# Kernel optimization log

Measured on AMD Instinct MI355X. Metric: run time of the kernel, lower is better.

Reference implementation:

```python
import jax, jax.numpy as jnp
import numpy as np

N = 50000
E = 800000
B = 8  # number of graphs


def gcn_conv(x, src, dst, W, b, n_nodes):
    # PyG GCNConv: add self-loops, symmetric deg^{-1/2} normalization,
    # linear transform, scatter-add aggregation at dst, then bias.
    loops = jnp.arange(n_nodes, dtype=src.dtype)
    s = jnp.concatenate([src, loops])
    d = jnp.concatenate([dst, loops])
    deg = jax.ops.segment_sum(jnp.ones_like(d, dtype=x.dtype), d, num_segments=n_nodes)
    dinv = jnp.where(deg > 0, jax.lax.rsqrt(deg), 0.0)
    norm = dinv[s] * dinv[d]                      # [E+N]
    xw = x @ W                                    # [N, out]
    msg = xw[s] * norm[:, None]                   # gather + scale
    out = jax.ops.segment_sum(msg, d, num_segments=n_nodes)  # scatter-add
    return out + b


def global_attention(x, batch, gate_w, gate_b, n_graphs):
    gate = x @ gate_w + gate_b                    # [N, 1]
    gmax = jax.ops.segment_max(gate, batch, num_segments=n_graphs)
    gmax = jnp.where(jnp.isfinite(gmax), gmax, 0.0)
    e = jnp.exp(gate - gmax[batch])               # segment-stable softmax
    denom = jax.ops.segment_sum(e, batch, num_segments=n_graphs)
    alpha = e / denom[batch]                      # [N, 1]
    return jax.ops.segment_sum(alpha * x, batch, num_segments=n_graphs)  # [B, d]


def setup_inputs() -> dict:
    key = jax.random.key(0)
    ks = jax.random.split(key, 10)
    x = jax.random.normal(ks[0], (N, 512), dtype=jnp.float32)
    edge_index = jax.random.randint(ks[1], (2, E), 0, N, dtype=jnp.int32)
    batch = jnp.sort(jax.random.randint(ks[2], (N,), 0, B, dtype=jnp.int32))
    W1 = jax.random.normal(ks[3], (512, 256), dtype=jnp.float32) / np.sqrt(512)
    b1 = jnp.zeros((256,), dtype=jnp.float32)
    W2 = jax.random.normal(ks[4], (256, 256), dtype=jnp.float32) / np.sqrt(256)
    b2 = jnp.zeros((256,), dtype=jnp.float32)
    gate_w = jax.random.normal(ks[5], (256, 1), dtype=jnp.float32) / np.sqrt(256)
    gate_b = jnp.zeros((1,), dtype=jnp.float32)
    return {"x": x, "edge_index": edge_index, "batch": batch,
            "W1": W1, "b1": b1, "W2": W2, "b2": b2,
            "gate_w": gate_w, "gate_b": gate_b}


def reference(x, edge_index, batch, W1, b1, W2, b2, gate_w, gate_b):
    src, dst = edge_index[0], edge_index[1]
    h = jax.nn.relu(gcn_conv(x, src, dst, W1, b1, N))
    h = jax.nn.relu(gcn_conv(h, src, dst, W2, b2, N))
    return global_attention(h, batch, gate_w, gate_b, B)
```

## Files before the change

kernel.cpp:

```cpp
#include <hip/hip_runtime.h>
#include <hip/hip_bf16.h>
#include <math.h>

#define FDIM 256
#define CAP 64
#define NGRAPH 8
#define GMAX_BLOCKS 64
#define FINAL_BLOCKS 512

typedef __attribute__((ext_vector_type(8))) short bf16x8;
typedef __attribute__((ext_vector_type(4))) float f32x4;
typedef __attribute__((ext_vector_type(2))) float f32x2;

__device__ __forceinline__ unsigned enc_f(float x){
  unsigned u = __float_as_uint(x);
  return (u >> 31) ? ~u : (u | 0x80000000u);
}
__device__ __forceinline__ float dec_f(unsigned u){
  return (u >> 31) ? __uint_as_float(u & 0x7FFFFFFFu) : __uint_as_float(~u);
}

__device__ __forceinline__ unsigned short f2bf(float f){
  unsigned u = __float_as_uint(f);
  unsigned r = (u + 0x7FFFu + ((u >> 16) & 1u)) >> 16;
  return (unsigned short)r;
}
__device__ __forceinline__ float bf2f(unsigned short h){
  return __uint_as_float(((unsigned)h) << 16);
}
__device__ __forceinline__ unsigned pk2(float a, float b){
  return (unsigned)f2bf(a) | ((unsigned)f2bf(b) << 16);
}
__device__ __forceinline__ unsigned char f2fp8(float v){
  unsigned p = __builtin_amdgcn_cvt_pk_fp8_f32(v, v, 0u, false);
  return (unsigned char)(p & 0xFFu);
}

__global__ void init_k(int* cnt, float* denom, float* out, int N){
  int i = blockIdx.x * blockDim.x + threadIdx.x;
  if (i < N) cnt[i] = 0;
  if (i < NGRAPH) denom[i] = 0.f;
  if (i < NGRAPH * FDIM) out[i] = 0.f;
}

__global__ void csr_k(const int* __restrict__ src, const int* __restrict__ dst,
                      int* __restrict__ cnt, int* __restrict__ col, int E){
  int e = blockIdx.x * blockDim.x + threadIdx.x;
  if (e < E){
    int d = dst[e];
    int pos = atomicAdd(&cnt[d], 1);
    if (pos < CAP) col[(size_t)d * CAP + pos] = src[e];
  }
}

__global__ void dinv_k(const int* __restrict__ cnt, float* __restrict__ dinv, int N){
  int i = blockIdx.x * blockDim.x + threadIdx.x;
  if (i < N) dinv[i] = rsqrtf((float)(cnt[i] + 1));
}

__global__ void wconv_k(const float* __restrict__ W1, const float* __restrict__ W2,
                        unsigned short* __restrict__ Wt1, unsigned short* __restrict__ Wt2){
  int idx = blockIdx.x * 256 + threadIdx.x;
  if (idx < 512 * 256){
    int k = idx >> 8, n = idx & 255;
    Wt1[(size_t)n * 512 + k] = f2bf(W1[idx]);
  } else {
    int j = idx - 512 * 256;
    if (j < 256 * 256){
      int k = j >> 8, n = j & 255;
      Wt2[(size_t)n * 256 + k] = f2bf(W2[j]);
    }
  }
}

template<int K, bool A_FP32>
__global__ __launch_bounds__(512) void gemm_k(const void* __restrict__ Av,
                                              const unsigned short* __restrict__ Bt,
                                              unsigned char* __restrict__ C, int M){
  __shared__ unsigned short As[128 * 64];
  __shared__ unsigned short Bs[256 * 64];
  const int tid = threadIdx.x;
  const int lane = tid & 63, wid = tid >> 6;
  const int wr = wid >> 2, wc = wid & 3;
  const int m0 = blockIdx.x * 128;
  f32x4 acc[4][4] = {};

  float4 arf0, arf1, arf2, arf3;
  uint4  arb0, arb1;
  uint4  brg0, brg1, brg2, brg3;

  const int rA0 = tid >> 3,          kqA0 = tid & 7;
  const int rA1 = (512 + tid) >> 3,  kqA1 = tid & 7;

  auto issue = [&](int k0){
    if (A_FP32){
      const float* A = (const float*)Av;
      const float* p0 = A + (size_t)min(m0 + rA0, M - 1) * K + k0 + kqA0 * 8;
      const float* p1 = A + (size_t)min(m0 + rA1, M - 1) * K + k0 + kqA1 * 8;
      arf0 = *(const float4*)p0; arf1 = *(const float4*)(p0 + 4);
      arf2 = *(const float4*)p1; arf3 = *(const float4*)(p1 + 4);
    } else {
      const unsigned short* A = (const unsigned short*)Av;
      arb0 = *(const uint4*)(A + (size_t)min(m0 + rA0, M - 1) * K + k0 + kqA0 * 8);
      arb1 = *(const uint4*)(A + (size_t)min(m0 + rA1, M - 1) * K + k0 + kqA1 * 8);
    }
    {
      int n0 = tid >> 3, n1 = (512 + tid) >> 3, n2 = (1024 + tid) >> 3, n3 = (1536 + tid) >> 3;
      int kq = tid & 7;
      brg0 = *(const uint4*)(Bt + (size_t)n0 * K + k0 + kq * 8);
      brg1 = *(const uint4*)(Bt + (size_t)n1 * K + k0 + kq * 8);
      brg2 = *(const uint4*)(Bt + (size_t)n2 * K + k0 + kq * 8);
      brg3 = *(const uint4*)(Bt + (size_t)n3 * K + k0 + kq * 8);
    }
  };

  auto writeLDS = [&](){
    int kq = tid & 7;
    {
      uint4 u0, u1;
      if (A_FP32){
        u0.x = pk2(arf0.x, arf0.y); u0.y = pk2(arf0.z, arf0.w);
        u0.z = pk2(arf1.x, arf1.y); u0.w = pk2(arf1.z, arf1.w);
        u1.x = pk2(arf2.x, arf2.y); u1.y = pk2(arf2.z, arf2.w);
        u1.z = pk2(arf3.x, arf3.y); u1.w = pk2(arf3.z, arf3.w);
      } else { u0 = arb0; u1 = arb1; }
      *(uint4*)((char*)As + ((rA0 * 128 + kq * 16) ^ ((rA0 & 7) << 4))) = u0;
      *(uint4*)((char*)As + ((rA1 * 128 + kq * 16) ^ ((rA1 & 7) << 4))) = u1;
    }
    {
      int n0 = tid >> 3, n1 = (512 + tid) >> 3, n2 = (1024 + tid) >> 3, n3 = (1536 + tid) >> 3;
      *(uint4*)((char*)Bs + ((n0 * 128 + kq * 16) ^ ((n0 & 7) << 4))) = brg0;
      *(uint4*)((char*)Bs + ((n1 * 128 + kq * 16) ^ ((n1 & 7) << 4))) = brg1;
      *(uint4*)((char*)Bs + ((n2 * 128 + kq * 16) ^ ((n2 & 7) << 4))) = brg2;
      *(uint4*)((char*)Bs + ((n3 * 128 + kq * 16) ^ ((n3 & 7) << 4))) = brg3;
    }
  };

  issue(0);
  for (int k0 = 0; k0 < K; k0 += 64){
    writeLDS();
    __syncthreads();
    if (k0 + 64 < K) issue(k0 + 64);

    #pragma unroll
    for (int kk = 0; kk < 64; kk += 32){
      bf16x8 af[4], bfr[4];
      int kb = kk * 2 + ((lane >> 4) << 4);
      #pragma unroll
      for (int mi = 0; mi < 4; ++mi){
        int r = wr * 64 + mi * 16 + (lane & 15);
        af[mi] = *(bf16x8*)((char*)As + ((r * 128 + kb) ^ ((r & 7) << 4)));
      }
      #pragma unroll
      for (int ni = 0; ni < 4; ++ni){
        int n = wc * 64 + ni * 16 + (lane & 15);
        bfr[ni] = *(bf16x8*)((char*)Bs + ((n * 128 + kb) ^ ((n & 7) << 4)));
      }
      #pragma unroll
      for (int mi = 0; mi < 4; ++mi)
        #pragma unroll
        for (int ni = 0; ni < 4; ++ni)
          acc[mi][ni] = __builtin_amdgcn_mfma_f32_16x16x32_bf16(af[mi], bfr[ni], acc[mi][ni], 0, 0, 0);
    }
    __syncthreads();
  }

  #pragma unroll
  for (int mi = 0; mi < 4; ++mi){
    #pragma unroll
    for (int reg = 0; reg < 4; ++reg){
      int row = m0 + wr * 64 + mi * 16 + ((lane >> 4) << 2) + reg;
      if (row < M){
        #pragma unroll
        for (int ni = 0; ni < 4; ++ni){
          int colc = wc * 64 + ni * 16 + (lane & 15);
          C[(size_t)row * FDIM + colc] = f2fp8(acc[mi][ni][reg]);
        }
      }
    }
  }
}

template<bool GATE>
__global__ __launch_bounds__(256) void agg_k(const unsigned char* __restrict__ xw,
                                             const float* __restrict__ dinv,
                                             const int* __restrict__ col,
                                             const int* __restrict__ cnt,
                                             const float* __restrict__ bias,
                                             unsigned short* __restrict__ outb,
                                             const float* __restrict__ gw,
                                             const float* __restrict__ gb,
                                             float* __restrict__ gate, int N){
  int node = blockIdx.x * 4 + (threadIdx.x >> 6);
  if (node >= N) return;
  int lane = threadIdx.x & 63;
  float di = dinv[node];
  int n = min(cnt[node], CAP);
  int s = 0; float w = 0.f;
  if (lane < n){ s = col[(size_t)node * CAP + lane]; w = di * dinv[s]; }

  float a0, a1, a2, a3;
  {
    unsigned u = *(const unsigned*)(xw + (size_t)node * FDIM + lane * 4);
    f32x2 lo = __builtin_amdgcn_cvt_pk_f32_fp8(u, false);
    f32x2 hi = __builtin_amdgcn_cvt_pk_f32_fp8(u, true);
    float sw = di * di;
    a0 = sw * lo.x; a1 = sw * lo.y; a2 = sw * hi.x; a3 = sw * hi.y;
  }

  unsigned bufA[8], bufB[8];
  int nc = (n + 7) >> 3;

  auto loadChunk = [&](unsigned (&buf)[8], int c){
    #pragma unroll
    for (int j = 0; j < 8; ++j){
      int e = c * 8 + j;
      int se = __shfl(s, e);
      buf[j] = *(const unsigned*)(xw + (size_t)se * FDIM + lane * 4);
    }
  };
  auto consChunk = [&](unsigned (&buf)[8], int c){
    #pragma unroll
    for (int j = 0; j < 8; ++j){
      int e = c * 8 + j;
      float we = __shfl(w, e);
      f32x2 lo = __builtin_amdgcn_cvt_pk_f32_fp8(buf[j], false);
      f32x2 hi = __builtin_amdgcn_cvt_pk_f32_fp8(buf[j], true);
      a0 += we * lo.x; a1 += we * lo.y;
      a2 += we * hi.x; a3 += we * hi.y;
    }
  };

  if (nc > 0) loadChunk(bufA, 0);
  for (int c = 0; c < nc; ++c){
    if (c & 1){
      if (c + 1 < nc) loadChunk(bufA, c + 1);
      consChunk(bufB, c);
    } else {
      if (c + 1 < nc) loadChunk(bufB, c + 1);
      consChunk(bufA, c);
    }
  }

  float4 bv = *(const float4*)(bias + lane * 4);
  a0 = fmaxf(a0 + bv.x, 0.f); a1 = fmaxf(a1 + bv.y, 0.f);
  a2 = fmaxf(a2 + bv.z, 0.f); a3 = fmaxf(a3 + bv.w, 0.f);
  {
    ushort4 r = make_ushort4(f2bf(a0), f2bf(a1), f2bf(a2), f2bf(a3));
    *(ushort4*)(outb + (size_t)node * FDIM + lane * 4) = r;
  }
  if (GATE){
    float4 g = *(const float4*)(gw + lane * 4);
    float val = a0 * g.x + a1 * g.y + a2 * g.z + a3 * g.w;
    #pragma unroll
    for (int off = 32; off; off >>= 1) val += __shfl_down(val, off);
    if (lane == 0) gate[node] = val + gb[0];
  }
}

__global__ __launch_bounds__(256) void gmax_k(const float* __restrict__ gate,
                                              const int* __restrict__ batch,
                                              unsigned* __restrict__ pmax, int N){
  __shared__ unsigned smax[NGRAPH];
  int tid = threadIdx.x;
  if (tid < NGRAPH) smax[tid] = 0u;
  __syncthreads();
  int chunk = (N + gridDim.x - 1) / gridDim.x;
  int begin = blockIdx.x * chunk;
  int end = min(begin + chunk, N);
  int curg = -1; unsigned curm = 0u;
  for (int i = begin + tid; i < end; i += 256){
    int g = batch[i];
    unsigned v = enc_f(gate[i]);
    if (g != curg){
      if (curg >= 0) atomicMax(&smax[curg], curm);
      curg = g; curm = v;
    } else if (v > curm) curm = v;
  }
  if (curg >= 0) atomicMax(&smax[curg], curm);
  __syncthreads();
  if (tid < NGRAPH) pmax[blockIdx.x * NGRAPH + tid] = smax[tid];
}

__global__ __launch_bounds__(256) void denom_k(float* __restrict__ gate,
                                               const int* __restrict__ batch,
                                               const unsigned* __restrict__ pmax,
                                               float* __restrict__ denom, int N){
  __shared__ unsigned sge[NGRAPH];
  __shared__ float gm[NGRAPH];
  __shared__ float dsum[NGRAPH];
  int tid = threadIdx.x;
  if (tid < NGRAPH){ sge[tid] = 0u; dsum[tid] = 0.f; }
  __syncthreads();
  for (int j = tid; j < GMAX_BLOCKS * NGRAPH; j += 256)
    atomicMax(&sge[j & (NGRAPH - 1)], pmax[j]);
  __syncthreads();
  if (tid < NGRAPH){
    unsigned u = sge[tid];
    gm[tid] = (u == 0u) ? 0.f : dec_f(u);
  }
  __syncthreads();
  int chunk = (N + gridDim.x - 1) / gridDim.x;
  int begin = blockIdx.x * chunk;
  int end = min(begin + chunk, N);
  int curg = -1; float cursum = 0.f;
  for (int i = begin + tid; i < end; i += 256){
    int g = batch[i];
    float e = expf(gate[i] - gm[g]);
    gate[i] = e;
    if (g != curg){
      if (curg >= 0) atomicAdd(&dsum[curg], cursum);
      curg = g; cursum = e;
    } else cursum += e;
  }
  if (curg >= 0) atomicAdd(&dsum[curg], cursum);
  __syncthreads();
  if (tid < NGRAPH && dsum[tid] != 0.f) atomicAdd(&denom[tid], dsum[tid]);
}

__global__ __launch_bounds__(256) void final_k(const unsigned short* __restrict__ h,
                                               const float* __restrict__ e,
                                               const int* __restrict__ batch,
                                               const float* __restrict__ denom,
                                               float* __restrict__ out, int N){
  __shared__ float sacc[NGRAPH * FDIM];
  int tid = threadIdx.x;
  #pragma unroll
  for (int j = tid; j < NGRAPH * FDIM; j += 256) sacc[j] = 0.f;
  __syncthreads();
  int lane = tid & 63, w = tid >> 6;
  int chunk = (N + gridDim.x - 1) / gridDim.x;
  int begin = blockIdx.x * chunk;
  int end = min(begin + chunk, N);
  float4 acc = make_float4(0.f, 0.f, 0.f, 0.f);
  int curg = -1;
  for (int i = begin + w; i < end; i += 4){
    int g = batch[i];
    if (g != curg){
      if (curg >= 0){
        atomicAdd(&sacc[curg * FDIM + lane * 4 + 0], acc.x);
        atomicAdd(&sacc[curg * FDIM + lane * 4 + 1], acc.y);
        atomicAdd(&sacc[curg * FDIM + lane * 4 + 2], acc.z);
        atomicAdd(&sacc[curg * FDIM + lane * 4 + 3], acc.w);
        acc = make_float4(0.f, 0.f, 0.f, 0.f);
      }
      curg = g;
    }
    float alpha = e[i] / denom[g];
    ushort4 v = *(const ushort4*)(h + (size_t)i * FDIM + lane * 4);
    acc.x += alpha * bf2f(v.x); acc.y += alpha * bf2f(v.y);
    acc.z += alpha * bf2f(v.z); acc.w += alpha * bf2f(v.w);
  }
  if (curg >= 0){
    atomicAdd(&sacc[curg * FDIM + lane * 4 + 0], acc.x);
    atomicAdd(&sacc[curg * FDIM + lane * 4 + 1], acc.y);
    atomicAdd(&sacc[curg * FDIM + lane * 4 + 2], acc.z);
    atomicAdd(&sacc[curg * FDIM + lane * 4 + 3], acc.w);
  }
  __syncthreads();
  if (begin < end){
    int g0 = batch[begin], g1 = batch[end - 1];
    for (int g = g0; g <= g1; ++g){
      float v = sacc[g * FDIM + tid];
      if (v != 0.f) atomicAdd(&out[g * FDIM + tid], v);
    }
  }
}

extern "C" void kernel_launch(void* const* d_in, const int* in_sizes, int n_in,
                              void* d_out, int out_size, void* d_ws, size_t ws_size,
                              hipStream_t stream){
  const float* x     = (const float*)d_in[0];
  const int*   ei    = (const int*)  d_in[1];
  const int*   batch = (const int*)  d_in[2];
  const float* W1    = (const float*)d_in[3];
  const float* b1    = (const float*)d_in[4];
  const float* W2    = (const float*)d_in[5];
  const float* b2    = (const float*)d_in[6];
  const float* gw    = (const float*)d_in[7];
  const float* gb    = (const float*)d_in[8];
  float* out = (float*)d_out;

  const int N = in_sizes[2];
  const int E = in_sizes[1] / 2;
  const int* src = ei;
  const int* dst = ei + E;

  size_t off = 0;
  auto carve = [&](size_t bytes) -> void* {
    void* p = (char*)d_ws + off;
    off += (bytes + 255) / 256 * 256;
    return p;
  };
  unsigned short* h     = (unsigned short*)carve((size_t)N * FDIM * 2);
  unsigned short* h1b   = (unsigned short*)carve((size_t)N * FDIM * 2);
  unsigned char*  xwb   = (unsigned char*) carve((size_t)N * FDIM);
  int*            cnt   = (int*)           carve((size_t)N * 4);
  float*          dinv  = (float*)         carve((size_t)N * 4);
  int*            col   = (int*)           carve((size_t)N * CAP * 4);
  float*          gate  = (float*)         carve((size_t)N * 4);
  unsigned*       pmax  = (unsigned*)      carve(GMAX_BLOCKS * NGRAPH * 4);
  float*          denom = (float*)         carve(NGRAPH * 4);
  unsigned short* Wt1   = (unsigned short*)carve((size_t)256 * 512 * 2);
  unsigned short* Wt2   = (unsigned short*)carve((size_t)256 * 256 * 2);
  (void)ws_size; (void)n_in; (void)out_size;

  const int TB = 256;
  init_k<<<(N + TB - 1) / TB, TB, 0, stream>>>(cnt, denom, out, N);
  csr_k<<<(E + TB - 1) / TB, TB, 0, stream>>>(src, dst, cnt, col, E);
  dinv_k<<<(N + TB - 1) / TB, TB, 0, stream>>>(cnt, dinv, N);
  wconv_k<<<(512 * 256 + 256 * 256 + TB - 1) / TB, TB, 0, stream>>>(W1, W2, Wt1, Wt2);

  int gblocks = (N + 127) / 128;
  int ablocks = (N + 3) / 4;
  gemm_k<512, true ><<<gblocks, 512, 0, stream>>>(x,   Wt1, xwb, N);
  agg_k<false><<<ablocks, 256, 0, stream>>>(xwb, dinv, col, cnt, b1, h1b, nullptr, nullptr, nullptr, N);
  gemm_k<256, false><<<gblocks, 512, 0, stream>>>(h1b, Wt2, xwb, N);
  agg_k<true ><<<ablocks, 256, 0, stream>>>(xwb, dinv, col, cnt, b2, h, gw, gb, gate, N);

  gmax_k<<<GMAX_BLOCKS, 256, 0, stream>>>(gate, batch, pmax, N);
  denom_k<<<GMAX_BLOCKS, 256, 0, stream>>>(gate, batch, pmax, denom, N);
  final_k<<<FINAL_BLOCKS, 256, 0, stream>>>(h, gate, batch, denom, out, N);
}
```

Measured before the change: 226.7 us.

## Deepen GEMM global-load prefetch to two register stages

The GEMM main loop now keeps two sets of prefetch registers (A/B stages) and issues global loads two K-tiles ahead, alternating between them in a loop that advances by 128. The goal is to hide more global memory latency behind the MFMA compute. The cost is roughly double the prefetch register footprint, which may lower occupancy or cause spills. The loop also assumes K is a multiple of 128, which holds for K=512 and K=256.

```diff
diff --git a/kernel.cpp b/kernel.cpp
--- a/kernel.cpp
+++ b/kernel.cpp
@@ -85,63 +85,81 @@
   const int m0 = blockIdx.x * 128;
   f32x4 acc[4][4] = {};
 
-  float4 arf0, arf1, arf2, arf3;
-  uint4  arb0, arb1;
-  uint4  brg0, brg1, brg2, brg3;
-
-  const int rA0 = tid >> 3,          kqA0 = tid & 7;
-  const int rA1 = (512 + tid) >> 3,  kqA1 = tid & 7;
-
-  auto issue = [&](int k0){
+  float4 fa0, fa1, fa2, fa3, fb0, fb1, fb2, fb3;
+  uint4  ua0, ua1, ub0, ub1;
+  uint4  ba0, ba1, ba2, ba3, bb0, bb1, bb2, bb3;
+
+  const int rA0 = tid >> 3,          kqA = tid & 7;
+  const int rA1 = (512 + tid) >> 3;
+  const int nB0 = tid >> 3, nB1 = (512 + tid) >> 3, nB2 = (1024 + tid) >> 3, nB3 = (1536 + tid) >> 3;
+
+  auto issueA = [&](int k0){
     if (A_FP32){
       const float* A = (const float*)Av;
-      const float* p0 = A + (size_t)min(m0 + rA0, M - 1) * K + k0 + kqA0 * 8;
-      const float* p1 = A + (size_t)min(m0 + rA1, M - 1) * K + k0 + kqA1 * 8;
-      arf0 = *(const float4*)p0; arf1 = *(const float4*)(p0 + 4);
-      arf2 = *(const float4*)p1; arf3 = *(const float4*)(p1 + 4);
+      const float* p0 = A + (size_t)min(m0 + rA0, M - 1) * K + k0 + kqA * 8;
+      const float* p1 = A + (size_t)min(m0 + rA1, M - 1) * K + k0 + kqA * 8;
+      fa0 = *(const float4*)p0; fa1 = *(const float4*)(p0 + 4);
+      fa2 = *(const float4*)p1; fa3 = *(const float4*)(p1 + 4);
     } else {
       const unsigned short* A = (const unsigned short*)Av;
-      arb0 = *(const uint4*)(A + (size_t)min(m0 + rA0, M - 1) * K + k0 + kqA0 * 8);
-      arb1 = *(const uint4*)(A + (size_t)min(m0 + rA1, M - 1) * K + k0 + kqA1 * 8);
-    }
-    {
-      int n0 = tid >> 3, n1 = (512 + tid) >> 3, n2 = (1024 + tid) >> 3, n3 = (1536 + tid) >> 3;
-      int kq = tid & 7;
-      brg0 = *(const uint4*)(Bt + (size_t)n0 * K + k0 + kq * 8);
-      brg1 = *(const uint4*)(Bt + (size_t)n1 * K + k0 + kq * 8);
-      brg2 = *(const uint4*)(Bt + (size_t)n2 * K + k0 + kq * 8);
-      brg3 = *(const uint4*)(Bt + (size_t)n3 * K + k0 + kq * 8);
-    }
-  };
-
-  auto writeLDS = [&](){
-    int kq = tid & 7;
-    {
-      uint4 u0, u1;
-      if (A_FP32){
-        u0.x = pk2(arf0.x, arf0.y); u0.y = pk2(arf0.z, arf0.w);
-        u0.z = pk2(arf1.x, arf1.y); u0.w = pk2(arf1.z, arf1.w);
-        u1.x = pk2(arf2.x, arf2.y); u1.y = pk2(arf2.z, arf2.w);
-        u1.z = pk2(arf3.x, arf3.y); u1.w = pk2(arf3.z, arf3.w);
-      } else { u0 = arb0; u1 = arb1; }
-      *(uint4*)((char*)As + ((rA0 * 128 + kq * 16) ^ ((rA0 & 7) << 4))) = u0;
-      *(uint4*)((char*)As + ((rA1 * 128 + kq * 16) ^ ((rA1 & 7) << 4))) = u1;
-    }
-    {
-      int n0 = tid >> 3, n1 = (512 + tid) >> 3, n2 = (1024 + tid) >> 3, n3 = (1536 + tid) >> 3;
-      *(uint4*)((char*)Bs + ((n0 * 128 + kq * 16) ^ ((n0 & 7) << 4))) = brg0;
-      *(uint4*)((char*)Bs + ((n1 * 128 + kq * 16) ^ ((n1 & 7) << 4))) = brg1;
-      *(uint4*)((char*)Bs + ((n2 * 128 + kq * 16) ^ ((n2 & 7) << 4))) = brg2;
-      *(uint4*)((char*)Bs + ((n3 * 128 + kq * 16) ^ ((n3 & 7) << 4))) = brg3;
-    }
-  };
-
-  issue(0);
-  for (int k0 = 0; k0 < K; k0 += 64){
-    writeLDS();
-    __syncthreads();
-    if (k0 + 64 < K) issue(k0 + 64);
-
+      ua0 = *(const uint4*)(A + (size_t)min(m0 + rA0, M - 1) * K + k0 + kqA * 8);
+      ua1 = *(const uint4*)(A + (size_t)min(m0 + rA1, M - 1) * K + k0 + kqA * 8);
+    }
+    ba0 = *(const uint4*)(Bt + (size_t)nB0 * K + k0 + kqA * 8);
+    ba1 = *(const uint4*)(Bt + (size_t)nB1 * K + k0 + kqA * 8);
+    ba2 = *(const uint4*)(Bt + (size_t)nB2 * K + k0 + kqA * 8);
+    ba3 = *(const uint4*)(Bt + (size_t)nB3 * K + k0 + kqA * 8);
+  };
+  auto issueB = [&](int k0){
+    if (A_FP32){
+      const float* A = (const float*)Av;
+      const float* p0 = A + (size_t)min(m0 + rA0, M - 1) * K + k0 + kqA * 8;
+      const float* p1 = A + (size_t)min(m0 + rA1, M - 1) * K + k0 + kqA * 8;
+      fb0 = *(const float4*)p0; fb1 = *(const float4*)(p0 + 4);
+      fb2 = *(const float4*)p1; fb3 = *(const float4*)(p1 + 4);
+    } else {
+      const unsigned short* A = (const unsigned short*)Av;
+      ub0 = *(const uint4*)(A + (size_t)min(m0 + rA0, M - 1) * K + k0 + kqA * 8);
+      ub1 = *(const uint4*)(A + (size_t)min(m0 + rA1, M - 1) * K + k0 + kqA * 8);
+    }
+    bb0 = *(const uint4*)(Bt + (size_t)nB0 * K + k0 + kqA * 8);
+    bb1 = *(const uint4*)(Bt + (size_t)nB1 * K + k0 + kqA * 8);
+    bb2 = *(const uint4*)(Bt + (size_t)nB2 * K + k0 + kqA * 8);
+    bb3 = *(const uint4*)(Bt + (size_t)nB3 * K + k0 + kqA * 8);
+  };
+
+  auto writeA = [&](){
+    uint4 u0, u1;
+    if (A_FP32){
+      u0.x = pk2(fa0.x, fa0.y); u0.y = pk2(fa0.z, fa0.w);
+      u0.z = pk2(fa1.x, fa1.y); u0.w = pk2(fa1.z, fa1.w);
+      u1.x = pk2(fa2.x, fa2.y); u1.y = pk2(fa2.z, fa2.w);
+      u1.z = pk2(fa3.x, fa3.y); u1.w = pk2(fa3.z, fa3.w);
+    } else { u0 = ua0; u1 = ua1; }
+    *(uint4*)((char*)As + ((rA0 * 128 + kqA * 16) ^ ((rA0 & 7) << 4))) = u0;
+    *(uint4*)((char*)As + ((rA1 * 128 + kqA * 16) ^ ((rA1 & 7) << 4))) = u1;
+    *(uint4*)((char*)Bs + ((nB0 * 128 + kqA * 16) ^ ((nB0 & 7) << 4))) = ba0;
+    *(uint4*)((char*)Bs + ((nB1 * 128 + kqA * 16) ^ ((nB1 & 7) << 4))) = ba1;
+    *(uint4*)((char*)Bs + ((nB2 * 128 + kqA * 16) ^ ((nB2 & 7) << 4))) = ba2;
+    *(uint4*)((char*)Bs + ((nB3 * 128 + kqA * 16) ^ ((nB3 & 7) << 4))) = ba3;
+  };
+  auto writeB = [&](){
+    uint4 u0, u1;
+    if (A_FP32){
+      u0.x = pk2(fb0.x, fb0.y); u0.y = pk2(fb0.z, fb0.w);
+      u0.z = pk2(fb1.x, fb1.y); u0.w = pk2(fb1.z, fb1.w);
+      u1.x = pk2(fb2.x, fb2.y); u1.y = pk2(fb2.z, fb2.w);
+      u1.z = pk2(fb3.x, fb3.y); u1.w = pk2(fb3.z, fb3.w);
+    } else { u0 = ub0; u1 = ub1; }
+    *(uint4*)((char*)As + ((rA0 * 128 + kqA * 16) ^ ((rA0 & 7) << 4))) = u0;
+    *(uint4*)((char*)As + ((rA1 * 128 + kqA * 16) ^ ((rA1 & 7) << 4))) = u1;
+    *(uint4*)((char*)Bs + ((nB0 * 128 + kqA * 16) ^ ((nB0 & 7) << 4))) = bb0;
+    *(uint4*)((char*)Bs + ((nB1 * 128 + kqA * 16) ^ ((nB1 & 7) << 4))) = bb1;
+    *(uint4*)((char*)Bs + ((nB2 * 128 + kqA * 16) ^ ((nB2 & 7) << 4))) = bb2;
+    *(uint4*)((char*)Bs + ((nB3 * 128 + kqA * 16) ^ ((nB3 & 7) << 4))) = bb3;
+  };
+
+  auto compute = [&](){
     #pragma unroll
     for (int kk = 0; kk < 64; kk += 32){
       bf16x8 af[4], bfr[4];
@@ -162,6 +180,20 @@
         for (int ni = 0; ni < 4; ++ni)
           acc[mi][ni] = __builtin_amdgcn_mfma_f32_16x16x32_bf16(af[mi], bfr[ni], acc[mi][ni], 0, 0, 0);
     }
+  };
+
+  issueA(0);
+  issueB(64);
+  for (int k0 = 0; k0 < K; k0 += 128){
+    writeA();
+    __syncthreads();
+    if (k0 + 128 < K) issueA(k0 + 128);
+    compute();
+    __syncthreads();
+    writeB();
+    __syncthreads();
+    if (k0 + 192 < K) issueB(k0 + 192);
+    compute();
     __syncthreads();
   }
 
```

After: 219.9 us. 3.0% less time.
